# Kernel optimization log

Hardware: AMD Instinct MI355X
Metric: run time of the kernel (lower is better)

Reference implementation:

```python
import jax, jax.numpy as jnp
import numpy as np

D = 4          # subsample stride for quantized refs
R = 6          # local search radius
P = 2 * R + 1  # 13
N = P * P      # 169
C = 32         # one-hot classes
BETA = 50.0
SIG = 1.0      # gaussian kernel sigma for kernel_soft_argmax
MPR = 12       # memory_patch_R
MPP = 2 * MPR + 1  # 25
DIL_INT = 15


def bilinear_gather(img, ys, xs):
    # img (b,c,h,w); ys,xs (b,n,h,w) float pixel coords; zero padding outside.
    b, c, h, w = img.shape
    y0f = jnp.floor(ys); x0f = jnp.floor(xs)
    wy = ys - y0f; wx = xs - x0f
    y0 = y0f.astype(jnp.int32); x0 = x0f.astype(jnp.int32)
    imgf = img.reshape(b, c, h * w)

    def corner(yi, xi, wgt):
        valid = (yi >= 0) & (yi < h) & (xi >= 0) & (xi < w)
        idx = jnp.clip(yi, 0, h - 1) * w + jnp.clip(xi, 0, w - 1)  # (b,n,h,w)
        g = jax.vmap(lambda f, ix: f[:, ix])(imgf, idx)            # (b,c,n,h,w)
        return g * (wgt * valid)[:, None]

    return (corner(y0, x0, (1 - wy) * (1 - wx))
            + corner(y0, x0 + 1, (1 - wy) * wx)
            + corner(y0 + 1, x0, wy * (1 - wx))
            + corner(y0 + 1, x0 + 1, wy * wx))


def deform_im2col(img, offset):
    # img (b,c,h,w); offset (b,h,w,2) ordered (dx,dy); returns (b,c,N,h,w)
    b, c, h, w = img.shape
    n = jnp.arange(N)
    dy = (n // P - R).astype(jnp.float32)
    dx = (n % P - R).astype(jnp.float32)
    yy = jnp.arange(h, dtype=jnp.float32)[:, None]
    xx = jnp.arange(w, dtype=jnp.float32)[None, :]
    ys = yy[None, None] + offset[..., 1][:, None] + dy[None, :, None, None]
    xs = xx[None, None] + offset[..., 0][:, None] + dx[None, :, None, None]
    return bilinear_gather(img, ys, xs)


def local_corr(t, r, rad, dil):
    # SpatialCorrelationSampler(kernel_size=1, patch_size=2*rad+1, dilation_patch=dil)
    pad = rad * dil
    rp = jnp.pad(r, ((0, 0), (0, 0), (pad, pad), (pad, pad)))
    offs = jnp.arange(2 * rad + 1) * dil

    def dot(oy, ox):
        rs = jax.lax.dynamic_slice(rp, (0, 0, oy, ox), t.shape)
        return jnp.sum(t * rs, axis=1)  # (b,h,w)

    f = jax.vmap(lambda oy: jax.vmap(lambda ox: dot(oy, ox))(offs))(offs)  # (Pp,Pp,b,h,w)
    return jnp.transpose(f, (2, 0, 1, 3, 4))  # (b,Pp,Pp,h,w), axis1=dy, axis2=dx


def unfold(x, ksz, pad):
    # torch F.unfold: (b,c,h,w) -> (b,c,ksz*ksz,h*w), n = ky*ksz+kx, zero pad
    b, c, h, w = x.shape
    xp = jnp.pad(x, ((0, 0), (0, 0), (pad, pad), (pad, pad)))
    offs = jnp.arange(ksz)
    sl = jax.vmap(lambda oy: jax.vmap(
        lambda ox: jax.lax.dynamic_slice(xp, (0, 0, oy, ox), x.shape))(offs))(offs)
    return jnp.transpose(sl, (2, 3, 0, 1, 4, 5)).reshape(b, c, ksz * ksz, h * w)


def kernel_soft_argmax(corr):
    # corr (B, N, h, w): gaussian-weight then softmax(beta * .) over N
    k = jnp.arange(P, dtype=jnp.float32)
    ctr = (P - 1) / 2.0
    g = jnp.exp(-(((k[None, :] - ctr) ** 2) + ((k[:, None] - ctr) ** 2)) / (2 * SIG ** 2))
    return jax.nn.softmax(BETA * (g.reshape(1, N, 1, 1) * corr), axis=1)


def get_grid(corr):
    # corr (B, N, h, w) -> soft-argmax grid (B, h, w, 2) in normalized coords
    B, n, h, w = corr.shape
    # replicate the torch meshgrid variable swap in the original get_grid
    x_map = jnp.broadcast_to(jnp.linspace(-1.0, 1.0, w)[None, :], (h, w)).astype(jnp.float32)
    y_map = jnp.broadcast_to(jnp.linspace(-1.0, 1.0, h)[:, None], (h, w)).astype(jnp.float32)
    xg = unfold(x_map[None, None], P, R)[:, 0]  # (1,N,hw)
    yg = unfold(y_map[None, None], P, R)[:, 0]
    wgt = corr.reshape(B, n, h * w)
    wgt = wgt / jnp.sum(wgt, 1, keepdims=True)
    gx = (wgt * xg).sum(1).reshape(B, h, w, 1)
    gy = (wgt * yg).sum(1).reshape(B, h, w, 1)
    return jnp.concatenate([gx, gy], 3)


def forward(feats_r, feats_t, quantized_r, ref_index, current_ind):
    ref_list = [int(v) for v in np.asarray(ref_index)]  # static config
    cur = int(current_ind)
    nref = feats_r.shape[0]
    nsearch = len([x for x in ref_list if cur - x > DIL_INT])
    dirates = [min(4, (cur - x) // DIL_INT + 1) for x in ref_list if cur - x > DIL_INT]
    b, c, h, w = feats_t.shape

    mdy = jnp.arange(-MPR, MPR + 1, dtype=jnp.float32)
    corrs, offsets = [], []
    for si in range(nsearch):
        cc = local_corr(feats_t, feats_r[si], MPR, dirates[si])       # (b,25,25,h,w)
        cc = jax.nn.softmax(cc.reshape(b, MPP * MPP, h * w), axis=1)
        cc = cc.reshape(b, MPP, MPP, h, w)
        offx = jnp.einsum('bpqhw,q->bhw', cc, mdy)   # expectation of dx
        offy = jnp.einsum('bpqhw,p->bhw', cc, mdy)   # expectation of dy
        off = jnp.stack([offx, offy], -1) * float(dirates[si])        # (b,h,w,2)
        offsets.append(off)
        col0 = deform_im2col(feats_r[si], off)                        # (b,c,N,h,w)
        corrs.append(jnp.einsum('bchw,bcnhw->bnhw', feats_t, col0))
    for ind in range(nsearch, nref):
        corrs.append(local_corr(feats_t, feats_r[ind], R, 1).reshape(b, N, h, w))

    corr = jnp.concatenate(corrs, 0)                 # (b*nref, N, h, w)
    corr = kernel_soft_argmax(corr)
    corr = corr.reshape(b, 1, N * nref, h * w)
    grid = get_grid(corr.reshape(-1, N, h, w))       # (b*nref, h, w, 2)

    # prep: subsample ::D and one-hot single-channel label maps
    labels = quantized_r[:, :, 0, ::D, ::D]          # (nref, b, h, w)
    qr = (labels[:, :, None] == jnp.arange(C)[None, None, :, None, None]).astype(jnp.float32)

    cols = []
    for i in range(nsearch):
        cols.append(deform_im2col(qr[i], offsets[i]).reshape(b, C, N, h * w))
    for i in range(nsearch, nref):
        cols.append(unfold(qr[i], P, R))
    image_uf = jnp.concatenate(cols, 2)              # (b, C, N*nref, hw)

    out = jnp.einsum('bnl,bcnl->bcl', corr[:, 0], image_uf).reshape(b, C, h, w)
    return out, grid


def setup_inputs() -> dict:
    key = jax.random.key(0)
    k1, k2, k3 = jax.random.split(key, 3)
    feats_r = jax.random.normal(k1, (3, 1, 64, 64, 64), dtype=jnp.float32)
    feats_t = jax.random.normal(k2, (1, 64, 64, 64), dtype=jnp.float32)
    quantized_r = jax.random.randint(k3, (3, 1, 1, 256, 256), 0, C, dtype=jnp.int32)
    return {
        'feats_r': feats_r,
        'feats_t': feats_t,
        'quantized_r': quantized_r,
        'ref_index': np.arange(3),
        'current_ind': 16,
    }


def reference(feats_r, feats_t, quantized_r, ref_index, current_ind):
    return forward(feats_r, feats_t, quantized_r, ref_index, current_ind)
```

## Files before the change

kernel.cpp:

```cpp
#include <hip/hip_runtime.h>


#define NPIX 4096

__device__ __forceinline__ float pdot8(float4 t0, float4 t1, float4 a,
                                       float4 b) {
  float s0 = t0.x * a.x, s1 = t0.y * a.y, s2 = t0.z * a.z, s3 = t0.w * a.w;
  s0 = fmaf(t1.x, b.x, s0);
  s1 = fmaf(t1.y, b.y, s1);
  s2 = fmaf(t1.z, b.z, s2);
  s3 = fmaf(t1.w, b.w, s3);
  return (s0 + s1) + (s2 + s3);
}

__device__ __forceinline__ float red8_4(float p0, float p1, float p2,
                                        float p3, int tx) {
  p0 += __shfl_xor(p0, 4);
  p1 += __shfl_xor(p1, 4);
  p2 += __shfl_xor(p2, 4);
  p3 += __shfl_xor(p3, 4);
  int t2 = tx & 3;
  bool o1 = t2 & 1, o2 = t2 & 2;
  float x01 = __shfl_xor(o1 ? p0 : p1, 1);
  float x23 = __shfl_xor(o1 ? p2 : p3, 1);
  float sA = (o1 ? p1 : p0) + x01;
  float sB = (o1 ? p3 : p2) + x23;
  float z = __shfl_xor(o2 ? sA : sB, 2);
  return o2 ? (sB + z) : (sA + z);
}

__device__ __forceinline__ float red8(float v) {
  v += __shfl_xor(v, 1);
  v += __shfl_xor(v, 2);
  v += __shfl_xor(v, 4);
  return v;
}

__device__ __forceinline__ float wredmax(float v) {
#pragma unroll
  for (int o = 32; o; o >>= 1) v = fmaxf(v, __shfl_down(v, o));
  return __shfl(v, 0);
}
__device__ __forceinline__ float wredsum(float v) {
#pragma unroll
  for (int o = 32; o; o >>= 1) v += __shfl_down(v, o);
  return __shfl(v, 0);
}

__global__ __launch_bounds__(256) void k_transpose(
    const float* __restrict__ ft, const float* __restrict__ fr,
    const int* __restrict__ q, float* __restrict__ tT, float* __restrict__ rT,
    unsigned char* __restrict__ lblp, float* __restrict__ out) {
  __shared__ float tile[64][65];
  int img = blockIdx.y;
  int pixBase = blockIdx.x * 64;
  const float* src = (img == 0) ? ft : fr + (img - 1) * (64 * NPIX);
  float* dst = (img == 0) ? tT : rT + (img - 1) * (64 * NPIX);
  int tid = threadIdx.x;
#pragma unroll
  for (int it = 0; it < 4; ++it) {
    int idx = it * 256 + tid;
    int c = idx >> 4;
    int p4 = (idx & 15) << 2;
    float4 v = *(const float4*)&src[c * NPIX + pixBase + p4];
    tile[p4 + 0][c] = v.x;
    tile[p4 + 1][c] = v.y;
    tile[p4 + 2][c] = v.z;
    tile[p4 + 3][c] = v.w;
  }
  __syncthreads();
#pragma unroll
  for (int it = 0; it < 4; ++it) {
    int idx = it * 256 + tid;
    int p = idx >> 4;
    int c4 = (idx & 15) << 2;
    float4 v = make_float4(tile[p][c4], tile[p][c4 + 1], tile[p][c4 + 2],
                           tile[p][c4 + 3]);
    *(float4*)&dst[(pixBase + p) * 64 + c4] = v;
  }
  if (img >= 1 && tid < 64) {
    int pix = pixBase + tid;
    lblp[(img - 1) * 4096 + pix] = (unsigned char)
        q[(img - 1) * 65536 + (pix >> 6) * 1024 + (pix & 63) * 4];
  }
  int gi = (blockIdx.y * 64 + blockIdx.x) * 256 + tid;
  out[gi] = 0.f;
  out[gi + 65536] = 0.f;
}

__global__ __launch_bounds__(256, 6) void k_fused(
    const float* __restrict__ tT, const float* __restrict__ rT,
    const unsigned char* __restrict__ lblp, float* __restrict__ out,
    float* __restrict__ grid) {
  int xg = blockIdx.x, y = blockIdx.y, z = blockIdx.z;
  int tid = threadIdx.x;
  int g = tid >> 3, tx = tid & 7;
  int w = tid >> 6, lane = tid & 63;

  __shared__ float cc1[4 * 636];
  __shared__ float D[4][196];
  __shared__ float P0[4][169];
  __shared__ float bins[4][33];

  if (tid < 132) ((float*)bins)[tid] = 0.f;

  int opix;

  if (z == 0) {
    int x0 = (xg >> 1) * 8 + (xg & 1);
    opix = x0;
    const float4* tb = (const float4*)&tT[((y << 6) + x0) << 6];
    float4 t0a = tb[0 * 32 + 2 * tx], t0b = tb[0 * 32 + 2 * tx + 1];
    float4 t1a = tb[1 * 32 + 2 * tx], t1b = tb[1 * 32 + 2 * tx + 1];
    float4 t2a = tb[2 * 32 + 2 * tx], t2b = tb[2 * 32 + 2 * tx + 1];
    float4 t3a = tb[3 * 32 + 2 * tx], t3b = tb[3 * 32 + 2 * tx + 1];

    {
      int u = g;
      int rx = x0 - 24 + 2 * u;
      bool cok = (unsigned)rx < 64u;
      int colB = min(max(rx, 0), 63) * 64 + tx * 8;
      int ox = u - (tx & 3);
      bool sok = (tx < 4) & ((unsigned)ox < 25u);
#pragma unroll 2
      for (int r = 0; r < 25; ++r) {
        int ry = y + 2 * r - 24;
        bool ok = cok & ((unsigned)ry < 64u);
        const float4* rp =
            (const float4*)&rT[min(max(ry, 0), 63) * 4096 + colB];
        float4 ra = rp[0], rb = rp[1];
        float v = red8_4(pdot8(t0a, t0b, ra, rb), pdot8(t1a, t1b, ra, rb),
                         pdot8(t2a, t2b, ra, rb), pdot8(t3a, t3b, ra, rb),
                         tx);
        v = ok ? v : 0.f;
        if (sok) cc1[(tx & 3) * 636 + r * 25 + ox] = v;
      }
    }
    __syncthreads();

    float offx, offy;
    {
      float vv[10];
      float m = -3e38f;
#pragma unroll
      for (int it = 0; it < 10; ++it) {
        unsigned o = lane + (it << 6);
        float v = (o < 625u) ? cc1[w * 636 + o] : -3e38f;
        vv[it] = v;
        m = fmaxf(m, v);
      }
      m = wredmax(m);
      float s = 0.f, sx = 0.f, sy = 0.f;
#pragma unroll
      for (int it = 0; it < 10; ++it) {
        unsigned o = lane + (it << 6);
        unsigned oy = o / 25u, ox = o - oy * 25u;
        float e = __expf(vv[it] - m);
        s += e;
        sx += e * (float)((int)ox - 12);
        sy += e * (float)((int)oy - 12);
      }
      s = wredsum(s);
      sx = wredsum(sx);
      sy = wredsum(sy);
      offx = 2.f * sx / s;
      offy = 2.f * sy / s;
    }

    float fy = floorf(offy), fx = floorf(offx);
    float wy = offy - fy, wx = offx - fx;
    float w00 = (1.f - wy) * (1.f - wx), w01 = (1.f - wy) * wx;
    float w10 = wy * (1.f - wx), w11 = wy * wx;
    int iy0 = y + (int)fy - 6;
    int ix0 = x0 + 2 * w + (int)fx - 6;

    {
      const float4* Tp = (const float4*)&tT[((y << 6) + x0 + 2 * w) << 6];
      float4 T0 = Tp[2 * tx], T1 = Tp[2 * tx + 1];
      int g3 = lane >> 3;
#pragma unroll 2
      for (int r = 0; r < 28; ++r) {
        int idx = g3 + (r << 3);
        int a = idx >> 4, b = idx & 15;
        int ry = iy0 + a, rx = ix0 + b;
        bool ok = (b < 14) & ((unsigned)ry < 64u) & ((unsigned)rx < 64u);
        const float4* rp = (const float4*)
            &rT[(min(max(ry, 0), 63) * 64 + min(max(rx, 0), 63)) * 64];
        float4 ra = rp[2 * tx], rb = rp[2 * tx + 1];
        float v = red8(pdot8(T0, T1, ra, rb));
        if (tx == 0 && b < 14) D[w][a * 14 + b] = ok ? v : 0.f;
      }
    }

    {
      int px = x0 + 2 * w, pix = (y << 6) + px;
      float sc[3];
      float m = -3e38f;
#pragma unroll
      for (int it = 0; it < 3; ++it) {
        unsigned o = lane + (it << 6);
        float scv = -3e38f;
        if (o < 169u) {
          unsigned i = o / 13u, j = o - i * 13u;
          float v = w00 * D[w][i * 14 + j] + w01 * D[w][i * 14 + j + 1] +
                    w10 * D[w][(i + 1) * 14 + j] +
                    w11 * D[w][(i + 1) * 14 + j + 1];
          float di = (float)(((int)i - 6) * ((int)i - 6) +
                             ((int)j - 6) * ((int)j - 6));
          scv = 50.f * __expf(-0.5f * di) * v;
        }
        sc[it] = scv;
        m = fmaxf(m, scv);
      }
      m = wredmax(m);
      float ee[3];
      float s = 0.f, gx = 0.f, gy = 0.f;
#pragma unroll
      for (int it = 0; it < 3; ++it) {
        unsigned o = lane + (it << 6);
        unsigned i = o / 13u, j = o - i * 13u;
        float e = __expf(sc[it] - m);
        ee[it] = e;
        int yy = y + (int)i - 6, xx = px + (int)j - 6;
        bool inb = (o < 169u) && (unsigned)yy < 64u && (unsigned)xx < 64u;
        s += e;
        gx += e * (inb ? (-1.f + (2.f / 63.f) * (float)xx) : 0.f);
        gy += e * (inb ? (-1.f + (2.f / 63.f) * (float)yy) : 0.f);
      }
      s = wredsum(s);
      gx = wredsum(gx);
      gy = wredsum(gy);
      float invS = 1.f / s;
#pragma unroll
      for (int it = 0; it < 3; ++it) {
        unsigned o = lane + (it << 6);
        if (o < 169u) P0[w][o] = ee[it] * invS;
      }
      if (lane == 0) {
        grid[pix * 2 + 0] = gx * invS;
        grid[pix * 2 + 1] = gy * invS;
      }
    }

    {
#pragma unroll
      for (int it = 0; it < 4; ++it) {
        int idx = lane + (it << 6);
        int a = idx >> 4, b = idx & 15;
        if (a < 14 && b < 14) {
          int ry = iy0 + a, rx = ix0 + b;
          if ((unsigned)ry < 64u && (unsigned)rx < 64u) {
            float wgt = 0.f;
            const float* crp = P0[w];
            if (a < 13) {
              if (b < 13) wgt = fmaf(w00, crp[a * 13 + b], wgt);
              if (b > 0) wgt = fmaf(w01, crp[a * 13 + b - 1], wgt);
            }
            if (a > 0) {
              if (b < 13) wgt = fmaf(w10, crp[(a - 1) * 13 + b], wgt);
              if (b > 0) wgt = fmaf(w11, crp[(a - 1) * 13 + b - 1], wgt);
            }
            if (wgt != 0.f) atomicAdd(&bins[w][lblp[ry * 64 + rx]], wgt);
          }
        }
      }
    }
    __syncthreads();
  } else {
    int k = z;
    int x0c = xg * 4;
    opix = -x0c - 1;
    const float* rb0 = rT + (k << 18);
    float (*cc2)[169] = (float(*)[169])cc1;
    const float4* tb = (const float4*)&tT[((y << 6) + x0c) << 6];
    float4 t0a = tb[0 * 16 + 2 * tx], t0b = tb[0 * 16 + 2 * tx + 1];
    float4 t1a = tb[1 * 16 + 2 * tx], t1b = tb[1 * 16 + 2 * tx + 1];
    float4 t2a = tb[2 * 16 + 2 * tx], t2b = tb[2 * 16 + 2 * tx + 1];
    float4 t3a = tb[3 * 16 + 2 * tx], t3b = tb[3 * 16 + 2 * tx + 1];

    {
#pragma unroll 2
      for (int r = 0; r < 7; ++r) {
        int idx = g + (r << 5);
        int i = idx >> 4, u = idx & 15;
        int ry = y + i - 6, rx = x0c - 6 + u;
        bool ok = (i < 13) & ((unsigned)ry < 64u) & ((unsigned)rx < 64u);
        const float4* rp = (const float4*)
            &rb0[min(max(ry, 0), 63) * 4096 + min(max(rx, 0), 63) * 64 +
                 tx * 8];
        float4 ra = rp[0], rb = rp[1];
        float v = red8_4(pdot8(t0a, t0b, ra, rb), pdot8(t1a, t1b, ra, rb),
                         pdot8(t2a, t2b, ra, rb), pdot8(t3a, t3b, ra, rb),
                         tx);
        v = ok ? v : 0.f;
        int j = u - (tx & 3);
        if ((tx < 4) && (i < 13) && ((unsigned)j < 13u))
          cc2[tx & 3][i * 13 + j] = v;
      }
    }
    __syncthreads();

    {
      int px = x0c + w, pix = (y << 6) + px;
      float sc[3];
      float m = -3e38f;
#pragma unroll
      for (int it = 0; it < 3; ++it) {
        unsigned o = lane + (it << 6);
        float scv = -3e38f;
        if (o < 169u) {
          unsigned i = o / 13u, j = o - i * 13u;
          float di = (float)(((int)i - 6) * ((int)i - 6) +
                             ((int)j - 6) * ((int)j - 6));
          scv = 50.f * __expf(-0.5f * di) * cc2[w][o];
        }
        sc[it] = scv;
        m = fmaxf(m, scv);
      }
      m = wredmax(m);
      float ee[3];
      float s = 0.f, gx = 0.f, gy = 0.f;
#pragma unroll
      for (int it = 0; it < 3; ++it) {
        unsigned o = lane + (it << 6);
        unsigned i = o / 13u, j = o - i * 13u;
        float e = __expf(sc[it] - m);
        ee[it] = e;
        int yy = y + (int)i - 6, xx = px + (int)j - 6;
        bool inb = (o < 169u) && (unsigned)yy < 64u && (unsigned)xx < 64u;
        s += e;
        gx += e * (inb ? (-1.f + (2.f / 63.f) * (float)xx) : 0.f);
        gy += e * (inb ? (-1.f + (2.f / 63.f) * (float)yy) : 0.f);
      }
      s = wredsum(s);
      gx = wredsum(gx);
      gy = wredsum(gy);
      float invS = 1.f / s;
#pragma unroll
      for (int it = 0; it < 3; ++it) {
        unsigned o = lane + (it << 6);
        if (o < 169u) {
          unsigned i = o / 13u, j = o - i * 13u;
          int yy = y + (int)i - 6, xx = px + (int)j - 6;
          if ((unsigned)yy < 64u && (unsigned)xx < 64u)
            atomicAdd(&bins[w][lblp[(k << 12) + yy * 64 + xx]],
                      ee[it] * invS);
        }
      }
      if (lane == 0) {
        grid[(k * NPIX + pix) * 2 + 0] = gx * invS;
        grid[(k * NPIX + pix) * 2 + 1] = gy * invS;
      }
    }
    __syncthreads();
  }

  if (tid < 128) {
    int pp = tid & 3, c = tid >> 2;
    int px = (opix >= 0) ? (opix + 2 * pp) : (-opix - 1 + pp);
    atomicAdd(&out[c * NPIX + (y << 6) + px], bins[pp][c]);
  }
}

extern "C" void kernel_launch(void* const* d_in, const int* in_sizes, int n_in,
                              void* d_out, int out_size, void* d_ws,
                              size_t ws_size, hipStream_t stream) {
  const float* fr = (const float*)d_in[0];
  const float* ft = (const float*)d_in[1];
  const int* q = (const int*)d_in[2];
  float* out = (float*)d_out;
  float* grid = out + 32 * NPIX;

  float* ws = (float*)d_ws;
  float* tT = ws;
  float* rT = ws + 262144;
  unsigned char* lblp = (unsigned char*)(ws + 1048576);

  k_transpose<<<dim3(64, 4), 256, 0, stream>>>(ft, fr, q, tT, rT, lblp, out);
  k_fused<<<dim3(16, 64, 3), 256, 0, stream>>>(tT, rT, lblp, out, grid);
}
```

Before: 49.98 us.

## Split channel dot products across 4 lanes instead of 8 to halve shuffles

After: 61.26 us. +22.6%, slower.

```diff
diff --git a/kernel.cpp b/kernel.cpp
--- a/kernel.cpp
+++ b/kernel.cpp
@@ -3,24 +3,22 @@
 
 #define NPIX 4096
 
-__device__ __forceinline__ float pdot8(float4 t0, float4 t1, float4 a,
-                                       float4 b) {
+__device__ __forceinline__ float pdot16(float4 t0, float4 t1, float4 t2,
+                                        float4 t3, float4 a, float4 b,
+                                        float4 c, float4 d) {
   float s0 = t0.x * a.x, s1 = t0.y * a.y, s2 = t0.z * a.z, s3 = t0.w * a.w;
-  s0 = fmaf(t1.x, b.x, s0);
-  s1 = fmaf(t1.y, b.y, s1);
-  s2 = fmaf(t1.z, b.z, s2);
-  s3 = fmaf(t1.w, b.w, s3);
+  s0 = fmaf(t1.x, b.x, s0); s1 = fmaf(t1.y, b.y, s1);
+  s2 = fmaf(t1.z, b.z, s2); s3 = fmaf(t1.w, b.w, s3);
+  s0 = fmaf(t2.x, c.x, s0); s1 = fmaf(t2.y, c.y, s1);
+  s2 = fmaf(t2.z, c.z, s2); s3 = fmaf(t2.w, c.w, s3);
+  s0 = fmaf(t3.x, d.x, s0); s1 = fmaf(t3.y, d.y, s1);
+  s2 = fmaf(t3.z, d.z, s2); s3 = fmaf(t3.w, d.w, s3);
   return (s0 + s1) + (s2 + s3);
 }
 
-__device__ __forceinline__ float red8_4(float p0, float p1, float p2,
-                                        float p3, int tx) {
-  p0 += __shfl_xor(p0, 4);
-  p1 += __shfl_xor(p1, 4);
-  p2 += __shfl_xor(p2, 4);
-  p3 += __shfl_xor(p3, 4);
-  int t2 = tx & 3;
-  bool o1 = t2 & 1, o2 = t2 & 2;
+__device__ __forceinline__ float xpose_reduce4(float p0, float p1, float p2,
+                                               float p3, int tx) {
+  bool o1 = tx & 1, o2 = tx & 2;
   float x01 = __shfl_xor(o1 ? p0 : p1, 1);
   float x23 = __shfl_xor(o1 ? p2 : p3, 1);
   float sA = (o1 ? p1 : p0) + x01;
@@ -29,10 +27,9 @@
   return o2 ? (sB + z) : (sA + z);
 }
 
-__device__ __forceinline__ float red8(float v) {
+__device__ __forceinline__ float red4(float v) {
   v += __shfl_xor(v, 1);
   v += __shfl_xor(v, 2);
-  v += __shfl_xor(v, 4);
   return v;
 }
 
@@ -88,13 +85,13 @@
   out[gi + 65536] = 0.f;
 }
 
-__global__ __launch_bounds__(256, 6) void k_fused(
+__global__ __launch_bounds__(256, 4) void k_fused(
     const float* __restrict__ tT, const float* __restrict__ rT,
     const unsigned char* __restrict__ lblp, float* __restrict__ out,
     float* __restrict__ grid) {
   int xg = blockIdx.x, y = blockIdx.y, z = blockIdx.z;
   int tid = threadIdx.x;
-  int g = tid >> 3, tx = tid & 7;
+  int g4 = tid >> 2, tx = tid & 3;
   int w = tid >> 6, lane = tid & 63;
 
   __shared__ float cc1[4 * 636];
@@ -110,30 +107,39 @@
     int x0 = (xg >> 1) * 8 + (xg & 1);
     opix = x0;
     const float4* tb = (const float4*)&tT[((y << 6) + x0) << 6];
-    float4 t0a = tb[0 * 32 + 2 * tx], t0b = tb[0 * 32 + 2 * tx + 1];
-    float4 t1a = tb[1 * 32 + 2 * tx], t1b = tb[1 * 32 + 2 * tx + 1];
-    float4 t2a = tb[2 * 32 + 2 * tx], t2b = tb[2 * 32 + 2 * tx + 1];
-    float4 t3a = tb[3 * 32 + 2 * tx], t3b = tb[3 * 32 + 2 * tx + 1];
-
-    {
-      int u = g;
-      int rx = x0 - 24 + 2 * u;
-      bool cok = (unsigned)rx < 64u;
-      int colB = min(max(rx, 0), 63) * 64 + tx * 8;
-      int ox = u - (tx & 3);
-      bool sok = (tx < 4) & ((unsigned)ox < 25u);
+    float4 t00 = tb[0 * 32 + 4 * tx + 0], t01 = tb[0 * 32 + 4 * tx + 1],
+           t02 = tb[0 * 32 + 4 * tx + 2], t03 = tb[0 * 32 + 4 * tx + 3];
+    float4 t10 = tb[1 * 32 + 4 * tx + 0], t11 = tb[1 * 32 + 4 * tx + 1],
+           t12 = tb[1 * 32 + 4 * tx + 2], t13 = tb[1 * 32 + 4 * tx + 3];
+    float4 t20 = tb[2 * 32 + 4 * tx + 0], t21 = tb[2 * 32 + 4 * tx + 1],
+           t22 = tb[2 * 32 + 4 * tx + 2], t23 = tb[2 * 32 + 4 * tx + 3];
+    float4 t30 = tb[3 * 32 + 4 * tx + 0], t31 = tb[3 * 32 + 4 * tx + 1],
+           t32 = tb[3 * 32 + 4 * tx + 2], t33 = tb[3 * 32 + 4 * tx + 3];
+
+    {
+      int row = g4 / 28;
+      int col = g4 - row * 28;
 #pragma unroll 2
-      for (int r = 0; r < 25; ++r) {
-        int ry = y + 2 * r - 24;
-        bool ok = cok & ((unsigned)ry < 64u);
-        const float4* rp =
-            (const float4*)&rT[min(max(ry, 0), 63) * 4096 + colB];
-        float4 ra = rp[0], rb = rp[1];
-        float v = red8_4(pdot8(t0a, t0b, ra, rb), pdot8(t1a, t1b, ra, rb),
-                         pdot8(t2a, t2b, ra, rb), pdot8(t3a, t3b, ra, rb),
-                         tx);
+      for (int r = 0; r < 11; ++r) {
+        bool rowok = row < 25;
+        int rx = x0 - 24 + 2 * col;
+        int ry = y + 2 * row - 24;
+        bool ok = rowok & ((unsigned)rx < 64u) & ((unsigned)ry < 64u);
+        const float4* rp = (const float4*)
+            &rT[min(max(ry, 0), 63) * 4096 + min(max(rx, 0), 63) * 64 +
+                tx * 16];
+        float4 ra = rp[0], rb = rp[1], rc = rp[2], rd = rp[3];
+        float p0 = pdot16(t00, t01, t02, t03, ra, rb, rc, rd);
+        float p1 = pdot16(t10, t11, t12, t13, ra, rb, rc, rd);
+        float p2 = pdot16(t20, t21, t22, t23, ra, rb, rc, rd);
+        float p3 = pdot16(t30, t31, t32, t33, ra, rb, rc, rd);
+        float v = xpose_reduce4(p0, p1, p2, p3, tx);
         v = ok ? v : 0.f;
-        if (sok) cc1[(tx & 3) * 636 + r * 25 + ox] = v;
+        int ox = col - tx;
+        if (rowok && (unsigned)ox < 25u) cc1[tx * 636 + row * 25 + ox] = v;
+        row += 2;
+        col += 8;
+        if (col >= 28) { col -= 28; ++row; }
       }
     }
     __syncthreads();
@@ -176,19 +182,19 @@
 
     {
       const float4* Tp = (const float4*)&tT[((y << 6) + x0 + 2 * w) << 6];
-      float4 T0 = Tp[2 * tx], T1 = Tp[2 * tx + 1];
-      int g3 = lane >> 3;
+      float4 T0 = Tp[4 * tx], T1 = Tp[4 * tx + 1], T2 = Tp[4 * tx + 2],
+             T3 = Tp[4 * tx + 3];
+      int b = lane >> 2;
 #pragma unroll 2
-      for (int r = 0; r < 28; ++r) {
-        int idx = g3 + (r << 3);
-        int a = idx >> 4, b = idx & 15;
-        int ry = iy0 + a, rx = ix0 + b;
+      for (int r = 0; r < 14; ++r) {
+        int ry = iy0 + r, rx = ix0 + b;
         bool ok = (b < 14) & ((unsigned)ry < 64u) & ((unsigned)rx < 64u);
         const float4* rp = (const float4*)
-            &rT[(min(max(ry, 0), 63) * 64 + min(max(rx, 0), 63)) * 64];
-        float4 ra = rp[2 * tx], rb = rp[2 * tx + 1];
-        float v = red8(pdot8(T0, T1, ra, rb));
-        if (tx == 0 && b < 14) D[w][a * 14 + b] = ok ? v : 0.f;
+            &rT[(min(max(ry, 0), 63) * 64 + min(max(rx, 0), 63)) * 64 +
+                tx * 16];
+        float4 ra = rp[0], rb = rp[1], rc = rp[2], rd = rp[3];
+        float v = red4(pdot16(T0, T1, T2, T3, ra, rb, rc, rd));
+        if (tx == 0 && b < 14) D[w][r * 14 + b] = ok ? v : 0.f;
       }
     }
 
@@ -273,29 +279,34 @@
     const float* rb0 = rT + (k << 18);
     float (*cc2)[169] = (float(*)[169])cc1;
     const float4* tb = (const float4*)&tT[((y << 6) + x0c) << 6];
-    float4 t0a = tb[0 * 16 + 2 * tx], t0b = tb[0 * 16 + 2 * tx + 1];
-    float4 t1a = tb[1 * 16 + 2 * tx], t1b = tb[1 * 16 + 2 * tx + 1];
-    float4 t2a = tb[2 * 16 + 2 * tx], t2b = tb[2 * 16 + 2 * tx + 1];
-    float4 t3a = tb[3 * 16 + 2 * tx], t3b = tb[3 * 16 + 2 * tx + 1];
+    float4 t00 = tb[0 * 16 + 4 * tx + 0], t01 = tb[0 * 16 + 4 * tx + 1],
+           t02 = tb[0 * 16 + 4 * tx + 2], t03 = tb[0 * 16 + 4 * tx + 3];
+    float4 t10 = tb[1 * 16 + 4 * tx + 0], t11 = tb[1 * 16 + 4 * tx + 1],
+           t12 = tb[1 * 16 + 4 * tx + 2], t13 = tb[1 * 16 + 4 * tx + 3];
+    float4 t20 = tb[2 * 16 + 4 * tx + 0], t21 = tb[2 * 16 + 4 * tx + 1],
+           t22 = tb[2 * 16 + 4 * tx + 2], t23 = tb[2 * 16 + 4 * tx + 3];
+    float4 t30 = tb[3 * 16 + 4 * tx + 0], t31 = tb[3 * 16 + 4 * tx + 1],
+           t32 = tb[3 * 16 + 4 * tx + 2], t33 = tb[3 * 16 + 4 * tx + 3];
 
     {
 #pragma unroll 2
-      for (int r = 0; r < 7; ++r) {
-        int idx = g + (r << 5);
+      for (int r = 0; r < 4; ++r) {
+        int idx = g4 + (r << 6);
         int i = idx >> 4, u = idx & 15;
         int ry = y + i - 6, rx = x0c - 6 + u;
         bool ok = (i < 13) & ((unsigned)ry < 64u) & ((unsigned)rx < 64u);
         const float4* rp = (const float4*)
             &rb0[min(max(ry, 0), 63) * 4096 + min(max(rx, 0), 63) * 64 +
-                 tx * 8];
-        float4 ra = rp[0], rb = rp[1];
-        float v = red8_4(pdot8(t0a, t0b, ra, rb), pdot8(t1a, t1b, ra, rb),
-                         pdot8(t2a, t2b, ra, rb), pdot8(t3a, t3b, ra, rb),
-                         tx);
+                 tx * 16];
+        float4 ra = rp[0], rb = rp[1], rc = rp[2], rd = rp[3];
+        float p0 = pdot16(t00, t01, t02, t03, ra, rb, rc, rd);
+        float p1 = pdot16(t10, t11, t12, t13, ra, rb, rc, rd);
+        float p2 = pdot16(t20, t21, t22, t23, ra, rb, rc, rd);
+        float p3 = pdot16(t30, t31, t32, t33, ra, rb, rc, rd);
+        float v = xpose_reduce4(p0, p1, p2, p3, tx);
         v = ok ? v : 0.f;
-        int j = u - (tx & 3);
-        if ((tx < 4) && (i < 13) && ((unsigned)j < 13u))
-          cc2[tx & 3][i * 13 + j] = v;
+        int j = u - tx;
+        if ((i < 13) && ((unsigned)j < 13u)) cc2[tx][i * 13 + j] = v;
       }
     }
     __syncthreads();
```
